# Performance work log

Measured on AMD Instinct MI355X. Metric: run time of the kernel, lower is better.

Reference implementation:

```python
import jax, jax.numpy as jnp
import numpy as np

H = 90          # hidden size
T = 240         # timesteps
F = 180         # encoder input features (3*60)


def _lstmcell_zero_state(x, W_ih, b_ih, b_hh):
    """nn.LSTMCell applied with h0=c0=0 (as in the original loops).
    x: [..., in_feat]; W_ih: [4H, in_feat]. Gate order i,f,g,o (PyTorch)."""
    gates = jnp.einsum('btf,gf->btg', x, W_ih) + b_ih + b_hh  # [B,T,4H]
    i, f, g, o = jnp.split(gates, 4, axis=-1)
    c = jax.nn.sigmoid(i) * jnp.tanh(g)          # f * c0 term vanishes (c0=0)
    return jax.nn.sigmoid(o) * jnp.tanh(c)       # h'


def setup_inputs() -> dict:
    key = jax.random.key(0)
    ks = jax.random.split(key, 9)
    s_enc = 1.0 / np.sqrt(H)
    inp = {
        'x': jax.random.normal(ks[0], (1024, 3, 60, T), dtype=jnp.float32),
        'enc_W_ih': jax.random.uniform(ks[1], (4 * H, F), jnp.float32, -s_enc, s_enc),
        'enc_b_ih': jax.random.uniform(ks[2], (4 * H,), jnp.float32, -s_enc, s_enc),
        'enc_b_hh': jax.random.uniform(ks[3], (4 * H,), jnp.float32, -s_enc, s_enc),
        'dec_W_ih': jax.random.uniform(ks[4], (4 * H, H), jnp.float32, -s_enc, s_enc),
        'dec_b_ih': jax.random.uniform(ks[5], (4 * H,), jnp.float32, -s_enc, s_enc),
        'dec_b_hh': jax.random.uniform(ks[6], (4 * H,), jnp.float32, -s_enc, s_enc),
        'out_W': jax.random.uniform(ks[7], (40, T * H), jnp.float32, -1.0 / np.sqrt(T * H), 1.0 / np.sqrt(T * H)),
        'out_b': jax.random.uniform(ks[8], (40,), jnp.float32, -1.0 / np.sqrt(T * H), 1.0 / np.sqrt(T * H)),
    }
    return inp


def reference(x, enc_W_ih, enc_b_ih, enc_b_hh, dec_W_ih, dec_b_ih, dec_b_hh, out_W, out_b):
    # Encoder: [B,3,60,240] -> [B,240,180]
    xe = jnp.transpose(x, (0, 3, 1, 2)).reshape(-1, T, F)
    h1 = jax.nn.sigmoid(_lstmcell_zero_state(xe, enc_W_ih, enc_b_ih, enc_b_hh))  # [B,T,90]
    # Decoder: per-step LSTMCell (also zero-state each step)
    h2 = _lstmcell_zero_state(h1, dec_W_ih, dec_b_ih, dec_b_hh)  # [B,T,90]
    out = h2.reshape(-1, T * H) @ out_W.T + out_b                # [B,40]
    out = out.reshape(-1, 4, 10)
    return jax.nn.softmax(out, axis=2)
```

## Files before the change

### kernel.cpp

```cpp
#include <hip/hip_runtime.h>
#include <hip/hip_bf16.h>

#define TT 240

typedef __attribute__((ext_vector_type(8))) short bf16x8;
typedef __attribute__((ext_vector_type(4))) float f32x4;

static __device__ __forceinline__ short f2bf(float f) {
    union { float f; unsigned int u; } c; c.f = f;
    return (short)((c.u + 0x8000u) >> 16);
}
static __device__ __forceinline__ unsigned int cvtpk(float lo, float hi) {
    unsigned int r;
    asm("v_cvt_pk_bf16_f32 %0, %1, %2" : "=v"(r) : "v"(lo), "v"(hi));
    return r;
}
static __device__ __forceinline__ float fexp2(float x) { return __builtin_amdgcn_exp2f(x); }
static __device__ __forceinline__ float frcp(float x)  { return __builtin_amdgcn_rcpf(x); }
#define LOG2E 1.4426950408889634f
static __device__ __forceinline__ float sigm(float x)  { return frcp(1.f + fexp2(-LOG2E * x)); }
static __device__ __forceinline__ float tanh_(float x) { return 2.f * frcp(1.f + fexp2(-2.f * LOG2E * x)) - 1.f; }

__global__ __launch_bounds__(256) void k_prep(
    const float* __restrict__ outW, const float* __restrict__ encW,
    const float* __restrict__ decW,
    short* __restrict__ woutB, short* __restrict__ wencP, short* __restrict__ wdecP)
{
    int idx = blockIdx.x * 256 + threadIdx.x;
    if (idx < 129600) {
        int row = idx / 2700, v = idx - row * 2700;
        uint4 w = {0u, 0u, 0u, 0u};
        if (row < 40) {
            const float* s = outW + row * 21600 + v * 8;
            f32x4 a = *(const f32x4*)(s);
            f32x4 b = *(const f32x4*)(s + 4);
            w.x = cvtpk(a[0], a[1]); w.y = cvtpk(a[2], a[3]);
            w.z = cvtpk(b[0], b[1]); w.w = cvtpk(b[2], b[3]);
        }
        *(uint4*)(woutB + row * 21600 + v * 8) = w;
        return;
    }
    idx -= 129600;
    if (idx < 288 * 192) {
        int row = idx / 192, k = idx - row * 192;
        int gi = row / 96, h = row - gi * 96;
        float v = 0.f;
        if (h < 90 && k < 180) {
            int srow = (gi == 0 ? 0 : (gi == 1 ? 180 : 270)) + h;
            v = encW[srow * 180 + k];
        }
        wencP[idx] = f2bf(v);
        return;
    }
    idx -= 288 * 192;
    if (idx < 288 * 96) {
        int row = idx / 96, k = idx - row * 96;
        int gi = row / 96, h = row - gi * 96;
        float v = 0.f;
        if (h < 90 && k < 90) {
            int srow = (gi == 0 ? 0 : (gi == 1 ? 180 : 270)) + h;
            v = decW[srow * 90 + k];
        }
        wdecP[idx] = f2bf(v);
    }
}

static __device__ __forceinline__ void stage_tile(
    const float* __restrict__ xq, short (*__restrict__ Xn)[200],
    int fb1, int v1, int has2, int fb2, int v2)
{
    const float* p1 = xq + (fb1 * 4) * 240 + v1 * 4;
    f32x4 A0 = *(const f32x4*)(p1);
    f32x4 A1 = *(const f32x4*)(p1 + 240);
    f32x4 A2 = *(const f32x4*)(p1 + 480);
    f32x4 A3 = *(const f32x4*)(p1 + 720);
    f32x4 B0, B1, B2, B3;
    if (has2) {
        const float* p2 = xq + (fb2 * 4) * 240 + v2 * 4;
        B0 = *(const f32x4*)(p2);
        B1 = *(const f32x4*)(p2 + 240);
        B2 = *(const f32x4*)(p2 + 480);
        B3 = *(const f32x4*)(p2 + 720);
    }
    #pragma unroll
    for (int i = 0; i < 4; ++i) {
        uint2 w;
        w.x = cvtpk(A0[i], A1[i]);
        w.y = cvtpk(A2[i], A3[i]);
        *(uint2*)(&Xn[v1 * 4 + i][fb1 * 4]) = w;
    }
    if (has2) {
        #pragma unroll
        for (int i = 0; i < 4; ++i) {
            uint2 w;
            w.x = cvtpk(B0[i], B1[i]);
            w.y = cvtpk(B2[i], B3[i]);
            *(uint2*)(&Xn[v2 * 4 + i][fb2 * 4]) = w;
        }
    }
}

__global__ __launch_bounds__(384, 3) void k_ed(
    const float* __restrict__ x,
    const short* __restrict__ wencP, const short* __restrict__ wdecP,
    const float* __restrict__ eb_ih, const float* __restrict__ eb_hh,
    const float* __restrict__ db_ih, const float* __restrict__ db_hh,
    short* __restrict__ h2)
{
    __shared__ short X[2][64][200];
    const int tid  = threadIdx.x;
    const int lane = tid & 63;
    const int wv   = tid >> 6;
    const int b    = blockIdx.x;
    const int r15  = lane & 15;
    const int k8   = lane >> 4;
    const int rbase = k8 * 4;

    bf16x8 wfE[3][6];
    #pragma unroll
    for (int g = 0; g < 3; ++g) {
        const short* wp = wencP + (g * 96 + wv * 16 + r15) * 192 + k8 * 8;
        #pragma unroll
        for (int kk = 0; kk < 6; ++kk) wfE[g][kk] = *(const bf16x8*)(wp + kk * 32);
    }
    bf16x8 wfD[3][3];
    #pragma unroll
    for (int g = 0; g < 3; ++g) {
        const short* wp = wdecP + (g * 96 + wv * 16 + r15) * 96 + k8 * 8;
        #pragma unroll
        for (int kk = 0; kk < 3; ++kk) wfD[g][kk] = *(const bf16x8*)(wp + kk * 32);
    }

    const int h  = wv * 16 + r15;
    const int hc = (h < 90) ? h : 89;
    const float bIe = eb_ih[hc] + eb_hh[hc];
    const float bGe = eb_ih[180 + hc] + eb_hh[180 + hc];
    const float bOe = eb_ih[270 + hc] + eb_hh[270 + hc];
    const float bId = db_ih[hc] + db_hh[hc];
    const float bGd = db_ih[180 + hc] + db_hh[180 + hc];
    const float bOd = db_ih[270 + hc] + db_hh[270 + hc];

    for (int i = tid; i < 2000; i += 384) {
        int bi = (i >= 1000);
        int j  = i - bi * 1000;
        if (j < 400) {
            int r = j / 100, c = j - r * 100;
            *(unsigned int*)(&X[bi][60 + r][c * 2]) = 0u;
        } else {
            int jj = j - 400;
            int r = jj / 10, c = jj - r * 10;
            *(unsigned int*)(&X[bi][r][180 + c * 2]) = 0u;
        }
    }

    const int fb1 = tid / 15, v1 = tid - fb1 * 15;
    const int has2 = (tid < 291);
    const int t2 = tid + 384;
    const int fb2 = t2 / 15, v2 = t2 - fb2 * 15;
    const float* xb = x + (size_t)b * 43200;
    short* h2g = h2 + (size_t)b * 21600;

    stage_tile(xb, X[0], fb1, v1, has2, fb2, v2);

    int p = 0;
    #pragma unroll 1
    for (int q = 0; q < 4; ++q) {
        __syncthreads();
        short (*Xc)[200] = X[p];

        short h1v[16];
        #pragma unroll
        for (int rs = 0; rs < 4; ++rs) {
            f32x4 aI = {0.f,0.f,0.f,0.f}, aG = {0.f,0.f,0.f,0.f}, aO = {0.f,0.f,0.f,0.f};
            #pragma unroll
            for (int kk = 0; kk < 6; ++kk) {
                bf16x8 a = *(const bf16x8*)(&Xc[rs * 16 + r15][kk * 32 + k8 * 8]);
                aI = __builtin_amdgcn_mfma_f32_16x16x32_bf16(a, wfE[0][kk], aI, 0, 0, 0);
                aG = __builtin_amdgcn_mfma_f32_16x16x32_bf16(a, wfE[1][kk], aG, 0, 0, 0);
                aO = __builtin_amdgcn_mfma_f32_16x16x32_bf16(a, wfE[2][kk], aO, 0, 0, 0);
            }
            #pragma unroll
            for (int rg = 0; rg < 4; ++rg) {
                float c  = sigm(aI[rg] + bIe) * tanh_(aG[rg] + bGe);
                float hv = sigm(aO[rg] + bOe) * tanh_(c);
                h1v[rs * 4 + rg] = f2bf(sigm(hv));
            }
        }
        __syncthreads();

        #pragma unroll
        for (int j = 0; j < 16; ++j)
            Xc[(j >> 2) * 16 + rbase + (j & 3)][h] = h1v[j];

        if (q < 3)
            stage_tile(xb + (q + 1) * 60, X[p ^ 1], fb1, v1, has2, fb2, v2);

        __syncthreads();

        #pragma unroll
        for (int rs = 0; rs < 4; ++rs) {
            f32x4 aI = {0.f,0.f,0.f,0.f}, aG = {0.f,0.f,0.f,0.f}, aO = {0.f,0.f,0.f,0.f};
            #pragma unroll
            for (int kk = 0; kk < 3; ++kk) {
                bf16x8 a = *(const bf16x8*)(&Xc[rs * 16 + r15][kk * 32 + k8 * 8]);
                aI = __builtin_amdgcn_mfma_f32_16x16x32_bf16(a, wfD[0][kk], aI, 0, 0, 0);
                aG = __builtin_amdgcn_mfma_f32_16x16x32_bf16(a, wfD[1][kk], aG, 0, 0, 0);
                aO = __builtin_amdgcn_mfma_f32_16x16x32_bf16(a, wfD[2][kk], aO, 0, 0, 0);
            }
            if (h < 90) {
                #pragma unroll
                for (int rg = 0; rg < 4; ++rg) {
                    int row = rs * 16 + rbase + rg;
                    float c  = sigm(aI[rg] + bId) * tanh_(aG[rg] + bGd);
                    float o2 = sigm(aO[rg] + bOd) * tanh_(c);
                    if (row < 60) h2g[q * 5400 + row * 90 + h] = f2bf(o2);
                }
            }
        }
        p ^= 1;
    }
}

#define KSPLIT 45
#define KST    15
__global__ __launch_bounds__(256) void k_out(
    const short* __restrict__ h2, const short* __restrict__ woutB,
    float* __restrict__ part, int B)
{
    __shared__ short Bs[48][488];
    const int MT  = B >> 6;
    const int bid = blockIdx.x;
    const int kc  = bid / MT;
    const int mt  = bid - kc * MT;
    const int tid = threadIdx.x;

    {
        const int k0 = kc * 480;
        #pragma unroll
        for (int j = 0; j < 12; ++j) {
            int g = tid + 256 * j;
            if (g < 2880) {
                int r = g / 60, c = g - r * 60;
                *(uint4*)(&Bs[r][c * 8]) =
                    *(const uint4*)(woutB + (size_t)r * 21600 + k0 + c * 8);
            }
        }
    }
    __syncthreads();

    const int w = tid >> 6, lane = tid & 63;
    const int r15 = lane & 15, k8 = lane >> 4;
    const int row = mt * 64 + w * 16 + r15;
    const short* aB = h2 + (size_t)row * 21600 + kc * 480 + k8 * 8;

    f32x4 a0 = {0.f,0.f,0.f,0.f}, a1 = {0.f,0.f,0.f,0.f}, a2 = {0.f,0.f,0.f,0.f};
    #pragma unroll
    for (int ks = 0; ks < KST; ++ks) {
        bf16x8 a  = *(const bf16x8*)(aB + ks * 32);
        bf16x8 q0 = *(const bf16x8*)(&Bs[r15][ks * 32 + k8 * 8]);
        bf16x8 q1 = *(const bf16x8*)(&Bs[16 + r15][ks * 32 + k8 * 8]);
        bf16x8 q2 = *(const bf16x8*)(&Bs[32 + r15][ks * 32 + k8 * 8]);
        a0 = __builtin_amdgcn_mfma_f32_16x16x32_bf16(a, q0, a0, 0, 0, 0);
        a1 = __builtin_amdgcn_mfma_f32_16x16x32_bf16(a, q1, a1, 0, 0, 0);
        a2 = __builtin_amdgcn_mfma_f32_16x16x32_bf16(a, q2, a2, 0, 0, 0);
    }
    float* pb = part + ((size_t)kc * B + mt * 64 + w * 16) * 48;
    #pragma unroll
    for (int rg = 0; rg < 4; ++rg) {
        int r = k8 * 4 + rg;
        pb[r * 48 +      r15] = a0[rg];
        pb[r * 48 + 16 + r15] = a1[rg];
        pb[r * 48 + 32 + r15] = a2[rg];
    }
}

__global__ __launch_bounds__(256) void k_soft(
    const float* __restrict__ part, const float* __restrict__ outb,
    float* __restrict__ out, int B)
{
    const int b = blockIdx.x, tid = threadIdx.x;
    __shared__ f32x4 red[16][12];
    __shared__ float vals[48];
    if (tid < 192) {
        int j = tid / 12, g = tid - j * 12;
        f32x4 s = {0.f, 0.f, 0.f, 0.f};
        for (int kc = j; kc < KSPLIT; kc += 16)
            s += *(const f32x4*)(part + ((size_t)kc * B + b) * 48 + g * 4);
        red[j][g] = s;
    }
    __syncthreads();
    if (tid < 12) {
        f32x4 s = red[0][tid];
        #pragma unroll
        for (int j = 1; j < 16; ++j) s += red[j][tid];
        #pragma unroll
        for (int e = 0; e < 4; ++e) {
            int o = tid * 4 + e;
            vals[o] = s[e] + ((o < 40) ? outb[o] : 0.f);
        }
    }
    __syncthreads();
    if (tid < 4) {
        float mx = -1e30f;
        #pragma unroll
        for (int j = 0; j < 10; ++j) mx = fmaxf(mx, vals[tid * 10 + j]);
        float e[10], s = 0.f;
        #pragma unroll
        for (int j = 0; j < 10; ++j) { e[j] = fexp2(LOG2E * (vals[tid * 10 + j] - mx)); s += e[j]; }
        float inv = frcp(s);
        #pragma unroll
        for (int j = 0; j < 10; ++j) out[b * 40 + tid * 10 + j] = e[j] * inv;
    }
}

extern "C" void kernel_launch(void* const* d_in, const int* in_sizes, int n_in,
                              void* d_out, int out_size, void* d_ws, size_t ws_size,
                              hipStream_t stream)
{
    const float* x     = (const float*)d_in[0];
    const float* encW  = (const float*)d_in[1];
    const float* eb_ih = (const float*)d_in[2];
    const float* eb_hh = (const float*)d_in[3];
    const float* decW  = (const float*)d_in[4];
    const float* db_ih = (const float*)d_in[5];
    const float* db_hh = (const float*)d_in[6];
    const float* outW  = (const float*)d_in[7];
    const float* outb  = (const float*)d_in[8];
    float* out = (float*)d_out;

    const int B = in_sizes[0] / (3 * 60 * TT);

    char* ws = (char*)d_ws;
    short* woutB = (short*)ws;
    short* wencP = (short*)(ws + 2073600);
    short* wdecP = (short*)(ws + 2184192);
    short* h2    = (short*)(ws + 2239488);
    float* part  = (float*)(ws + 2239488 + (size_t)B * 43200);

    k_prep<<<dim3(831), dim3(256), 0, stream>>>(outW, encW, decW, woutB, wencP, wdecP);
    k_ed<<<dim3(B), dim3(384), 0, stream>>>(x, wencP, wdecP, eb_ih, eb_hh,
                                            db_ih, db_hh, h2);
    k_out<<<dim3(KSPLIT * (B >> 6)), dim3(256), 0, stream>>>(h2, woutB, part, B);
    k_soft<<<dim3(B), dim3(256), 0, stream>>>(part, outb, out, B);
}
```

Measured before the change: 374.0 us.

## Split encoder-decoder kernel into one block per 60-step chunk

The k_ed kernel previously ran one block per batch element and looped over four 60-timestep chunks, double-buffering the input tile in shared memory. Now each block handles a single chunk, so the grid grows fourfold and the loop, the double buffer and the prefetch are gone. Shared memory per block is halved, and weights are loaded per gate just before use rather than kept in registers for the whole kernel, which lowers register pressure. The cost is that every block reloads the encoder and decoder weight fragments, and there is no longer any in-block overlap between staging the next tile and computing the current one.

```diff
diff --git a/kernel.cpp b/kernel.cpp
--- a/kernel.cpp
+++ b/kernel.cpp
@@ -65,41 +65,6 @@
     }
 }
 
-static __device__ __forceinline__ void stage_tile(
-    const float* __restrict__ xq, short (*__restrict__ Xn)[200],
-    int fb1, int v1, int has2, int fb2, int v2)
-{
-    const float* p1 = xq + (fb1 * 4) * 240 + v1 * 4;
-    f32x4 A0 = *(const f32x4*)(p1);
-    f32x4 A1 = *(const f32x4*)(p1 + 240);
-    f32x4 A2 = *(const f32x4*)(p1 + 480);
-    f32x4 A3 = *(const f32x4*)(p1 + 720);
-    f32x4 B0, B1, B2, B3;
-    if (has2) {
-        const float* p2 = xq + (fb2 * 4) * 240 + v2 * 4;
-        B0 = *(const f32x4*)(p2);
-        B1 = *(const f32x4*)(p2 + 240);
-        B2 = *(const f32x4*)(p2 + 480);
-        B3 = *(const f32x4*)(p2 + 720);
-    }
-    #pragma unroll
-    for (int i = 0; i < 4; ++i) {
-        uint2 w;
-        w.x = cvtpk(A0[i], A1[i]);
-        w.y = cvtpk(A2[i], A3[i]);
-        *(uint2*)(&Xn[v1 * 4 + i][fb1 * 4]) = w;
-    }
-    if (has2) {
-        #pragma unroll
-        for (int i = 0; i < 4; ++i) {
-            uint2 w;
-            w.x = cvtpk(B0[i], B1[i]);
-            w.y = cvtpk(B2[i], B3[i]);
-            *(uint2*)(&Xn[v2 * 4 + i][fb2 * 4]) = w;
-        }
-    }
-}
-
 __global__ __launch_bounds__(384, 3) void k_ed(
     const float* __restrict__ x,
     const short* __restrict__ wencP, const short* __restrict__ wdecP,
@@ -107,29 +72,15 @@
     const float* __restrict__ db_ih, const float* __restrict__ db_hh,
     short* __restrict__ h2)
 {
-    __shared__ short X[2][64][200];
+    __shared__ short Xc[64][200];
     const int tid  = threadIdx.x;
     const int lane = tid & 63;
     const int wv   = tid >> 6;
-    const int b    = blockIdx.x;
+    const int b    = blockIdx.x >> 2;
+    const int q    = blockIdx.x & 3;
     const int r15  = lane & 15;
     const int k8   = lane >> 4;
     const int rbase = k8 * 4;
-
-    bf16x8 wfE[3][6];
-    #pragma unroll
-    for (int g = 0; g < 3; ++g) {
-        const short* wp = wencP + (g * 96 + wv * 16 + r15) * 192 + k8 * 8;
-        #pragma unroll
-        for (int kk = 0; kk < 6; ++kk) wfE[g][kk] = *(const bf16x8*)(wp + kk * 32);
-    }
-    bf16x8 wfD[3][3];
-    #pragma unroll
-    for (int g = 0; g < 3; ++g) {
-        const short* wp = wdecP + (g * 96 + wv * 16 + r15) * 96 + k8 * 8;
-        #pragma unroll
-        for (int kk = 0; kk < 3; ++kk) wfD[g][kk] = *(const bf16x8*)(wp + kk * 32);
-    }
 
     const int h  = wv * 16 + r15;
     const int hc = (h < 90) ? h : 89;
@@ -140,84 +91,117 @@
     const float bGd = db_ih[180 + hc] + db_hh[180 + hc];
     const float bOd = db_ih[270 + hc] + db_hh[270 + hc];
 
-    for (int i = tid; i < 2000; i += 384) {
-        int bi = (i >= 1000);
-        int j  = i - bi * 1000;
-        if (j < 400) {
-            int r = j / 100, c = j - r * 100;
-            *(unsigned int*)(&X[bi][60 + r][c * 2]) = 0u;
+    for (int i = tid; i < 1000; i += 384) {
+        if (i < 400) {
+            int r = i / 100, c = i - r * 100;
+            *(unsigned int*)(&Xc[60 + r][c * 2]) = 0u;
         } else {
-            int jj = j - 400;
-            int r = jj / 10, c = jj - r * 10;
-            *(unsigned int*)(&X[bi][r][180 + c * 2]) = 0u;
-        }
-    }
-
-    const int fb1 = tid / 15, v1 = tid - fb1 * 15;
-    const int has2 = (tid < 291);
-    const int t2 = tid + 384;
-    const int fb2 = t2 / 15, v2 = t2 - fb2 * 15;
-    const float* xb = x + (size_t)b * 43200;
-    short* h2g = h2 + (size_t)b * 21600;
-
-    stage_tile(xb, X[0], fb1, v1, has2, fb2, v2);
-
-    int p = 0;
-    #pragma unroll 1
-    for (int q = 0; q < 4; ++q) {
-        __syncthreads();
-        short (*Xc)[200] = X[p];
-
-        short h1v[16];
+            int j = i - 400, r = j / 10, c = j - r * 10;
+            *(unsigned int*)(&Xc[r][180 + c * 2]) = 0u;
+        }
+    }
+
+    {
+        const float* xq = x + (size_t)b * 43200 + q * 60;
+        const int fb1 = tid / 15, v1 = tid - fb1 * 15;
+        {
+            const float* p = xq + (fb1 * 4) * 240 + v1 * 4;
+            f32x4 A0 = *(const f32x4*)(p);
+            f32x4 A1 = *(const f32x4*)(p + 240);
+            f32x4 A2 = *(const f32x4*)(p + 480);
+            f32x4 A3 = *(const f32x4*)(p + 720);
+            #pragma unroll
+            for (int i = 0; i < 4; ++i) {
+                uint2 w;
+                w.x = cvtpk(A0[i], A1[i]);
+                w.y = cvtpk(A2[i], A3[i]);
+                *(uint2*)(&Xc[v1 * 4 + i][fb1 * 4]) = w;
+            }
+        }
+        if (tid < 291) {
+            int t2 = tid + 384;
+            int fb2 = t2 / 15, v2 = t2 - fb2 * 15;
+            const float* p = xq + (fb2 * 4) * 240 + v2 * 4;
+            f32x4 A0 = *(const f32x4*)(p);
+            f32x4 A1 = *(const f32x4*)(p + 240);
+            f32x4 A2 = *(const f32x4*)(p + 480);
+            f32x4 A3 = *(const f32x4*)(p + 720);
+            #pragma unroll
+            for (int i = 0; i < 4; ++i) {
+                uint2 w;
+                w.x = cvtpk(A0[i], A1[i]);
+                w.y = cvtpk(A2[i], A3[i]);
+                *(uint2*)(&Xc[v2 * 4 + i][fb2 * 4]) = w;
+            }
+        }
+    }
+    __syncthreads();
+
+    f32x4 accE[3][4];
+    #pragma unroll
+    for (int g = 0; g < 3; ++g) {
+        bf16x8 wf[6];
+        const short* wp = wencP + (g * 96 + wv * 16 + r15) * 192 + k8 * 8;
+        #pragma unroll
+        for (int kk = 0; kk < 6; ++kk) wf[kk] = *(const bf16x8*)(wp + kk * 32);
         #pragma unroll
         for (int rs = 0; rs < 4; ++rs) {
-            f32x4 aI = {0.f,0.f,0.f,0.f}, aG = {0.f,0.f,0.f,0.f}, aO = {0.f,0.f,0.f,0.f};
+            f32x4 a4 = {0.f, 0.f, 0.f, 0.f};
             #pragma unroll
             for (int kk = 0; kk < 6; ++kk) {
                 bf16x8 a = *(const bf16x8*)(&Xc[rs * 16 + r15][kk * 32 + k8 * 8]);
-                aI = __builtin_amdgcn_mfma_f32_16x16x32_bf16(a, wfE[0][kk], aI, 0, 0, 0);
-                aG = __builtin_amdgcn_mfma_f32_16x16x32_bf16(a, wfE[1][kk], aG, 0, 0, 0);
-                aO = __builtin_amdgcn_mfma_f32_16x16x32_bf16(a, wfE[2][kk], aO, 0, 0, 0);
-            }
-            #pragma unroll
-            for (int rg = 0; rg < 4; ++rg) {
-                float c  = sigm(aI[rg] + bIe) * tanh_(aG[rg] + bGe);
-                float hv = sigm(aO[rg] + bOe) * tanh_(c);
-                h1v[rs * 4 + rg] = f2bf(sigm(hv));
-            }
-        }
-        __syncthreads();
-
-        #pragma unroll
-        for (int j = 0; j < 16; ++j)
-            Xc[(j >> 2) * 16 + rbase + (j & 3)][h] = h1v[j];
-
-        if (q < 3)
-            stage_tile(xb + (q + 1) * 60, X[p ^ 1], fb1, v1, has2, fb2, v2);
-
-        __syncthreads();
-
+                a4 = __builtin_amdgcn_mfma_f32_16x16x32_bf16(a, wf[kk], a4, 0, 0, 0);
+            }
+            accE[g][rs] = a4;
+        }
+    }
+    unsigned short h1v[16];
+    #pragma unroll
+    for (int rs = 0; rs < 4; ++rs) {
+        #pragma unroll
+        for (int rg = 0; rg < 4; ++rg) {
+            float c  = sigm(accE[0][rs][rg] + bIe) * tanh_(accE[1][rs][rg] + bGe);
+            float hv = sigm(accE[2][rs][rg] + bOe) * tanh_(c);
+            h1v[rs * 4 + rg] = (unsigned short)f2bf(sigm(hv));
+        }
+    }
+    __syncthreads();
+
+    #pragma unroll
+    for (int j = 0; j < 16; ++j)
+        Xc[(j >> 2) * 16 + rbase + (j & 3)][h] = (short)h1v[j];
+    __syncthreads();
+
+    f32x4 accD[3][4];
+    #pragma unroll
+    for (int g = 0; g < 3; ++g) {
+        bf16x8 wf[3];
+        const short* wp = wdecP + (g * 96 + wv * 16 + r15) * 96 + k8 * 8;
+        #pragma unroll
+        for (int kk = 0; kk < 3; ++kk) wf[kk] = *(const bf16x8*)(wp + kk * 32);
         #pragma unroll
         for (int rs = 0; rs < 4; ++rs) {
-            f32x4 aI = {0.f,0.f,0.f,0.f}, aG = {0.f,0.f,0.f,0.f}, aO = {0.f,0.f,0.f,0.f};
+            f32x4 a4 = {0.f, 0.f, 0.f, 0.f};
             #pragma unroll
             for (int kk = 0; kk < 3; ++kk) {
                 bf16x8 a = *(const bf16x8*)(&Xc[rs * 16 + r15][kk * 32 + k8 * 8]);
-                aI = __builtin_amdgcn_mfma_f32_16x16x32_bf16(a, wfD[0][kk], aI, 0, 0, 0);
-                aG = __builtin_amdgcn_mfma_f32_16x16x32_bf16(a, wfD[1][kk], aG, 0, 0, 0);
-                aO = __builtin_amdgcn_mfma_f32_16x16x32_bf16(a, wfD[2][kk], aO, 0, 0, 0);
-            }
-            if (h < 90) {
-                #pragma unroll
-                for (int rg = 0; rg < 4; ++rg) {
-                    int row = rs * 16 + rbase + rg;
-                    float c  = sigm(aI[rg] + bId) * tanh_(aG[rg] + bGd);
-                    float o2 = sigm(aO[rg] + bOd) * tanh_(c);
-                    if (row < 60) h2g[q * 5400 + row * 90 + h] = f2bf(o2);
-                }
-            }
-        }
-        p ^= 1;
+                a4 = __builtin_amdgcn_mfma_f32_16x16x32_bf16(a, wf[kk], a4, 0, 0, 0);
+            }
+            accD[g][rs] = a4;
+        }
+    }
+    if (h < 90) {
+        short* h2g = h2 + (size_t)b * 21600 + q * 5400;
+        #pragma unroll
+        for (int rs = 0; rs < 4; ++rs) {
+            #pragma unroll
+            for (int rg = 0; rg < 4; ++rg) {
+                int row = rs * 16 + rbase + rg;
+                float c  = sigm(accD[0][rs][rg] + bId) * tanh_(accD[1][rs][rg] + bGd);
+                float o2 = sigm(accD[2][rs][rg] + bOd) * tanh_(c);
+                if (row < 60) h2g[row * 90 + h] = f2bf(o2);
+            }
+        }
     }
 }
 
@@ -338,8 +322,8 @@
     float* part  = (float*)(ws + 2239488 + (size_t)B * 43200);
 
     k_prep<<<dim3(831), dim3(256), 0, stream>>>(outW, encW, decW, woutB, wencP, wdecP);
-    k_ed<<<dim3(B), dim3(384), 0, stream>>>(x, wencP, wdecP, eb_ih, eb_hh,
-                                            db_ih, db_hh, h2);
+    k_ed<<<dim3(B * 4), dim3(384), 0, stream>>>(x, wencP, wdecP, eb_ih, eb_hh,
+                                                db_ih, db_hh, h2);
     k_out<<<dim3(KSPLIT * (B >> 6)), dim3(256), 0, stream>>>(h2, woutB, part, B);
     k_soft<<<dim3(B), dim3(256), 0, stream>>>(part, outb, out, B);
 }
```

After: 369.8 us. No clear change (-1.1%).
